# Kernel optimization log

Hardware: AMD Instinct MI355X
Metric: run time of the kernel (lower is better)

Reference implementation:

```python
import jax, jax.numpy as jnp
import numpy as np


def setup_inputs() -> dict:
    key = jax.random.key(0)
    ks = jax.random.split(key, 8)
    B, N, D, H = 8, 512, 64, 64
    user_embeddings = jax.random.normal(ks[0], (B, N, D), dtype=jnp.float32)
    past_lengths = jax.random.randint(ks[1], (B,), 0, N)
    valid_mask = jnp.ones((B, N), dtype=jnp.float32)
    # MLP params: Linear(4D -> H), PReLU (single slope), Linear(H -> 1)
    s1 = 1.0 / np.sqrt(4 * D)
    s2 = 1.0 / np.sqrt(H)
    W1 = jax.random.uniform(ks[2], (H, 4 * D), minval=-s1, maxval=s1, dtype=jnp.float32)
    b1 = jax.random.uniform(ks[3], (H,), minval=-s1, maxval=s1, dtype=jnp.float32)
    prelu_a = jnp.float32(0.25)
    W2 = jax.random.uniform(ks[4], (1, H), minval=-s2, maxval=s2, dtype=jnp.float32)
    b2 = jax.random.uniform(ks[5], (1,), minval=-s2, maxval=s2, dtype=jnp.float32)
    return {"past_lengths": past_lengths, "user_embeddings": user_embeddings,
            "valid_mask": valid_mask, "W1": W1, "b1": b1, "prelu_a": prelu_a,
            "W2": W2, "b2": b2}


def reference(past_lengths, user_embeddings, valid_mask, W1, b1, prelu_a, W2, b2):
    # DIN local activation attention with causal mask.
    # Original math: h = W1 @ concat(Q, K, Q-K, Q*K) + b1 per (q,k) pair.
    # Split W1 into its 4 D-sized blocks so the concat tensor [B,N,N,4D] is
    # never materialized; the pairwise hidden [B,N,N,H] is the only big buffer.
    B, N, D = user_embeddings.shape
    Wq, Wk, Wd, Wm = jnp.split(W1, 4, axis=1)  # each [H, D]
    x = user_embeddings
    # Q and (Q-K)'s +Q part -> per-query term; K and (Q-K)'s -K part -> per-key term
    hq = jnp.einsum('bqd,hd->bqh', x, Wq + Wd)          # [B,N,H]
    hk = jnp.einsum('bkd,hd->bkh', x, Wk - Wd)          # [B,N,H]
    hm = jnp.einsum('bqd,bkd,hd->bqkh', x, x, Wm)       # [B,N,N,H] (Q*K term)
    h = hq[:, :, None, :] + hk[:, None, :, :] + hm + b1
    h = jnp.where(h > 0, h, prelu_a * h)                # PReLU
    scores = jnp.einsum('bqkh,h->bqk', h, W2[0]) + b2[0]  # [B,N,N]
    causal = jnp.tril(jnp.ones((N, N), dtype=scores.dtype))
    scores = scores * causal[None, :, :]
    scores = scores * valid_mask[:, None, :]            # key-side padding mask
    encoded = jnp.einsum('bqk,bkd->bqd', scores, x)     # weighted sum (no softmax)
    return encoded
```

## Files before the change

kernel.cpp:

```cpp
#include <hip/hip_runtime.h>

#define NB 8
#define NN 512

#define WS_WMF 0
#define WS_HQ  4096
#define WS_BF  266240
#define WS_XE  528384

typedef float fx4 __attribute__((ext_vector_type(4)));
typedef short sx8 __attribute__((ext_vector_type(8)));
typedef int   ix4 __attribute__((ext_vector_type(4)));

static __device__ inline unsigned short f2bf(float f) {
    unsigned u = __float_as_uint(f);
    return (unsigned short)((u + 0x7FFFu + ((u >> 16) & 1u)) >> 16);
}

static __device__ inline void async_cp16(const void* g, void* l) {
    __builtin_amdgcn_global_load_lds(
        (const __attribute__((address_space(1))) unsigned int*)g,
        (__attribute__((address_space(3))) unsigned int*)l, 16, 0, 0);
}

__global__ __launch_bounds__(256) void prep(const float* __restrict__ x,
                                            const float* __restrict__ vm,
                                            const float* __restrict__ W1,
                                            const float* __restrict__ b1,
                                            float* __restrict__ ws) {
    __shared__ float lwq[64 * 68];
    __shared__ float lwk[64 * 68];
    __shared__ float xs[1024];
    const int t = threadIdx.x;
    const int blk = blockIdx.x;

    {
        int d = t & 63, hb = t >> 6;
        #pragma unroll 4
        for (int i = 0; i < 16; ++i) {
            int h = i * 4 + hb;
            float a = W1[h * 256 + d];
            float bb = W1[h * 256 + 64 + d];
            float c = W1[h * 256 + 128 + d];
            lwq[h * 68 + d] = a + c;
            lwk[h * 68 + d] = bb - c;
        }
    }
    const int r0 = blk * 16;
    #pragma unroll
    for (int i = 0; i < 4; ++i)
        xs[i * 256 + t] = x[r0 * 64 + i * 256 + t];
    __syncthreads();

    {
        int r4 = t >> 6, h = t & 63;
        const fx4* wqv = (const fx4*)(lwq + h * 68);
        const fx4* wkv = (const fx4*)(lwk + h * 68);
        float bh = b1[h];
        unsigned short* bfp = (unsigned short*)(ws + WS_BF);
        #pragma unroll 1
        for (int g = 0; g < 4; ++g) {
            int r = g * 4 + r4;
            const fx4* xr = (const fx4*)(xs + r * 64);
            float aq = bh, ak = 0.f;
            #pragma unroll
            for (int dd = 0; dd < 16; ++dd) {
                fx4 xv = xr[dd];
                fx4 wq = wqv[dd];
                fx4 wk = wkv[dd];
                aq = fmaf(xv[0], wq[0], aq); aq = fmaf(xv[1], wq[1], aq);
                aq = fmaf(xv[2], wq[2], aq); aq = fmaf(xv[3], wq[3], aq);
                ak = fmaf(xv[0], wk[0], ak); ak = fmaf(xv[1], wk[1], ak);
                ak = fmaf(xv[2], wk[2], ak); ak = fmaf(xv[3], wk[3], ak);
            }
            int row = r0 + r;
            (ws + WS_HQ)[row * 64 + h] = aq;
            int bb = row >> 9, k = row & 511;
            int tt = k >> 4, nn = k & 15;
            int c = 2 + (h >> 5);
            int qd = (h >> 3) & 3, j = h & 7;
            int ln = qd * 16 + nn;
            bfp[((((bb * 32 + tt) * 4 + c) * 64 + ln) << 3) + j] = f2bf(ak);
        }
    }

    {
        int b = blk >> 5, t5 = blk & 31;
        if (t < 128) {
            unsigned short* bfp = (unsigned short*)(ws + WS_BF);
            int c = t >> 6, L = t & 63;
            int nn = L & 15, qd = L >> 4;
            const float* src = x + ((b * 512 + t5 * 16 + nn) * 64 + c * 32 + qd * 8);
            fx4 v0 = *(const fx4*)src;
            fx4 v1 = *(const fx4*)(src + 4);
            uint4 o;
            o.x = (unsigned)f2bf(v0[0]) | ((unsigned)f2bf(v0[1]) << 16);
            o.y = (unsigned)f2bf(v0[2]) | ((unsigned)f2bf(v0[3]) << 16);
            o.z = (unsigned)f2bf(v1[0]) | ((unsigned)f2bf(v1[1]) << 16);
            o.w = (unsigned)f2bf(v1[2]) | ((unsigned)f2bf(v1[3]) << 16);
            *(uint4*)(bfp + ((((b * 32 + t5) * 4 + c) * 64 + L) << 3)) = o;
        }
        {
            unsigned short* xep = (unsigned short*)(ws + WS_XE);
            int c32 = t5 >> 1, half = t5 & 1;
            int nt = t >> 6, r = t & 63;
            int L = half * 32 + (r & 31);
            int j0 = (r >> 5) * 4;
            int quad = L >> 4, nn = L & 15;
            unsigned short u[4];
            #pragma unroll
            for (int i = 0; i < 4; ++i) {
                int key = c32 * 32 + quad * 8 + j0 + i;
                float v = x[(b * 512 + key) * 64 + nt * 16 + nn] * vm[b * 512 + key];
                u[i] = f2bf(v);
            }
            uint2 o;
            o.x = (unsigned)u[0] | ((unsigned)u[1] << 16);
            o.y = (unsigned)u[2] | ((unsigned)u[3] << 16);
            *(uint2*)(xep + (((((b * 16 + c32) * 4 + nt) * 64 + L) << 3) + j0)) = o;
        }
    }
    if (blk < 2) {
        float* wmf = ws + WS_WMF;
        int e = blk * 256 + t;
        int slot = e >> 6, lane = e & 63;
        int ht = slot >> 1, hf = slot & 1;
        int mm = lane & 15, qd = lane >> 4;
        int h = ht * 16 + mm;
        int dbase = hf * 32 + qd * 8;
        #pragma unroll
        for (int j = 0; j < 8; ++j)
            wmf[e * 8 + j] = W1[h * 256 + 192 + dbase + j];
    }
}

__global__ __launch_bounds__(256, 2) void k2_main(const float* __restrict__ x,
                                                  const float* __restrict__ prelu_a,
                                                  const float* __restrict__ W2,
                                                  const float* __restrict__ b2,
                                                  const float* __restrict__ ws,
                                                  float* __restrict__ out) {
    const int tid  = threadIdx.x;
    const int lane = tid & 63;
    const int w    = tid >> 6;
    const int blk  = blockIdx.x;
    const int band = (int)((0x4501763298DCABEFULL >> ((blk >> 6) << 2)) & 0xF);
    const int rest = blk & 63;
    const int b    = rest >> 3;
    const int s    = rest & 7;
    const int n    = lane & 15, quad = lane >> 4;
    const int q    = band * 32 + s * 4 + w;
    const int bq   = b * 512 + q;
    const int cmax = band;

    const float* wmf = ws + WS_WMF;
    const float* hq  = ws + WS_HQ;
    const unsigned short* bfp = (const unsigned short*)(ws + WS_BF);
    const unsigned short* xep = (const unsigned short*)(ws + WS_XE);

    const float pa  = prelu_a[0];
    const float b2v = b2[0];

    __shared__ uint4 bufS[2][512];
    __shared__ unsigned strip[4][16];

    fx4 w2v[4];
    #pragma unroll
    for (int ht = 0; ht < 4; ++ht)
        w2v[ht] = *(const fx4*)(W2 + ht * 16 + quad * 4);
    sx8 oh[4];
    #pragma unroll
    for (int ht = 0; ht < 4; ++ht) {
        sx8 a;
        #pragma unroll
        for (int jj = 0; jj < 8; ++jj) {
            int hp = (ht >> 1) * 32 + quad * 8 + jj;
            a[jj] = (hp == ht * 16 + n) ? (short)0x3F80 : (short)0;
        }
        oh[ht] = a;
    }
    const unsigned sel = (quad < 2) ? 0x05040100u : 0x07060302u;

    fx4 hqv[4];
    #pragma unroll
    for (int ht = 0; ht < 4; ++ht)
        hqv[ht] = *(const fx4*)(hq + bq * 64 + ht * 16 + quad * 4);
    float xq[2][8];
    {
        const float* xp = x + bq * 64 + quad * 8;
        fx4 t0 = *(const fx4*)xp;
        fx4 t1 = *(const fx4*)(xp + 4);
        fx4 t2 = *(const fx4*)(xp + 32);
        fx4 t3 = *(const fx4*)(xp + 36);
        #pragma unroll
        for (int jj = 0; jj < 4; ++jj) {
            xq[0][jj] = t0[jj]; xq[0][4 + jj] = t1[jj];
            xq[1][jj] = t2[jj]; xq[1][4 + jj] = t3[jj];
        }
    }
    sx8 afrag[4][2];
    #pragma unroll
    for (int ht = 0; ht < 4; ++ht)
        #pragma unroll
        for (int hf = 0; hf < 2; ++hf) {
            const float* wp = wmf + (((ht * 2 + hf) * 64 + lane) << 3);
            fx4 w0 = *(const fx4*)wp;
            fx4 w1 = *(const fx4*)(wp + 4);
            sx8 a;
            #pragma unroll
            for (int jj = 0; jj < 4; ++jj) {
                a[jj]     = (short)f2bf(w0[jj] * xq[hf][jj]);
                a[4 + jj] = (short)f2bf(w1[jj] * xq[hf][4 + jj]);
            }
            afrag[ht][hf] = a;
        }

    fx4 eacc[4];
    #pragma unroll
    for (int nt = 0; nt < 4; ++nt) eacc[nt] = (fx4){0.f, 0.f, 0.f, 0.f};

    {
        const uint4* sS = (const uint4*)(bfp + (unsigned)(b * 32) * 2048);
        async_cp16(sS + tid,       &bufS[0][tid]);
        async_cp16(sS + tid + 256, &bufS[0][tid + 256]);
    }
    __syncthreads();

    #pragma unroll 1
    for (int c = 0; c <= cmax; ++c) {
        if (c < cmax) {
            const int p2 = (c + 1) & 1;
            const uint4* sS = (const uint4*)(bfp + (unsigned)(b * 32 + 2 * (c + 1)) * 2048);
            async_cp16(sS + tid,       &bufS[p2][tid]);
            async_cp16(sS + tid + 256, &bufS[p2][tid + 256]);
        }

        const int p = c & 1;
        const unsigned short* ls = (const unsigned short*)&bufS[p][0] + (lane << 3);
        sx8 fa0 = *(const sx8*)(ls);
        sx8 fa1 = *(const sx8*)(ls + 512);
        sx8 fa2 = *(const sx8*)(ls + 1024);
        sx8 fa3 = *(const sx8*)(ls + 1536);
        sx8 fb0 = *(const sx8*)(ls + 2048);
        sx8 fb1 = *(const sx8*)(ls + 2560);
        sx8 fb2 = *(const sx8*)(ls + 3072);
        sx8 fb3 = *(const sx8*)(ls + 3584);

        fx4 accA[4], accB[4];
        #pragma unroll
        for (int ht = 0; ht < 4; ++ht) { accA[ht] = hqv[ht]; accB[ht] = hqv[ht]; }
        #pragma unroll
        for (int ht = 0; ht < 4; ++ht) {
            accA[ht] = __builtin_amdgcn_mfma_f32_16x16x32_bf16(afrag[ht][0], fa0, accA[ht], 0, 0, 0);
            accB[ht] = __builtin_amdgcn_mfma_f32_16x16x32_bf16(afrag[ht][0], fb0, accB[ht], 0, 0, 0);
        }
        #pragma unroll
        for (int ht = 0; ht < 4; ++ht) {
            accA[ht] = __builtin_amdgcn_mfma_f32_16x16x32_bf16(afrag[ht][1], fa1, accA[ht], 0, 0, 0);
            accB[ht] = __builtin_amdgcn_mfma_f32_16x16x32_bf16(afrag[ht][1], fb1, accB[ht], 0, 0, 0);
        }
        #pragma unroll
        for (int ht = 0; ht < 4; ++ht) {
            accA[ht] = __builtin_amdgcn_mfma_f32_16x16x32_bf16(oh[ht], (ht < 2) ? fa2 : fa3, accA[ht], 0, 0, 0);
            accB[ht] = __builtin_amdgcn_mfma_f32_16x16x32_bf16(oh[ht], (ht < 2) ? fb2 : fb3, accB[ht], 0, 0, 0);
        }

        const unsigned short* le = xep + ((unsigned)(b * 16 + c) * 2048) + (lane << 3);
        sx8 e0 = *(const sx8*)(le);
        sx8 e1 = *(const sx8*)(le + 512);
        sx8 e2 = *(const sx8*)(le + 1024);
        sx8 e3 = *(const sx8*)(le + 1536);

        fx4 s0v = (fx4){0.f, 0.f, 0.f, 0.f};
        fx4 s1v = (fx4){0.f, 0.f, 0.f, 0.f};
        #pragma unroll
        for (int ht = 0; ht < 4; ++ht) {
            fx4 za = accA[ht], zb = accB[ht];
            fx4 ta = __builtin_elementwise_max(za, za * pa);
            fx4 tb = __builtin_elementwise_max(zb, zb * pa);
            s0v = ta * w2v[ht] + s0v;
            s1v = tb * w2v[ht] + s1v;
        }
        float s0 = (s0v[0] + s0v[1]) + (s0v[2] + s0v[3]);
        float s1 = (s1v[0] + s1v[1]) + (s1v[2] + s1v[3]);
        s0 += __shfl_xor(s0, 16, 64);
        s0 += __shfl_xor(s0, 32, 64);
        s1 += __shfl_xor(s1, 16, 64);
        s1 += __shfl_xor(s1, 32, 64);
        int k0 = c * 32 + n;
        s0 = (k0 <= q)      ? s0 + b2v : 0.f;
        s1 = (k0 + 16 <= q) ? s1 + b2v : 0.f;

        unsigned packed = (unsigned)f2bf(s0) | ((unsigned)f2bf(s1) << 16);
        if (quad == 0) strip[w][n] = packed;
        const unsigned* sp = &strip[w][(quad & 1) * 8];
        uint4 wv0 = *(const uint4*)sp;
        uint4 wv1 = *(const uint4*)(sp + 4);
        ix4 sw_;
        sw_[0] = (int)__builtin_amdgcn_perm(wv0.y, wv0.x, sel);
        sw_[1] = (int)__builtin_amdgcn_perm(wv0.w, wv0.z, sel);
        sw_[2] = (int)__builtin_amdgcn_perm(wv1.y, wv1.x, sel);
        sw_[3] = (int)__builtin_amdgcn_perm(wv1.w, wv1.z, sel);
        sx8 sfrag = __builtin_bit_cast(sx8, sw_);

        eacc[0] = __builtin_amdgcn_mfma_f32_16x16x32_bf16(sfrag, e0, eacc[0], 0, 0, 0);
        eacc[1] = __builtin_amdgcn_mfma_f32_16x16x32_bf16(sfrag, e1, eacc[1], 0, 0, 0);
        eacc[2] = __builtin_amdgcn_mfma_f32_16x16x32_bf16(sfrag, e2, eacc[2], 0, 0, 0);
        eacc[3] = __builtin_amdgcn_mfma_f32_16x16x32_bf16(sfrag, e3, eacc[3], 0, 0, 0);

        __syncthreads();
    }

    float ov = eacc[0][0];
    if (quad == 1) ov = eacc[1][0];
    if (quad == 2) ov = eacc[2][0];
    if (quad == 3) ov = eacc[3][0];
    out[bq * 64 + lane] = ov;
}

extern "C" void kernel_launch(void* const* d_in, const int* in_sizes, int n_in,
                              void* d_out, int out_size, void* d_ws, size_t ws_size,
                              hipStream_t stream) {
    const float* x   = (const float*)d_in[1];
    const float* vmk = (const float*)d_in[2];
    const float* W1  = (const float*)d_in[3];
    const float* b1  = (const float*)d_in[4];
    const float* pa  = (const float*)d_in[5];
    const float* W2  = (const float*)d_in[6];
    const float* b2  = (const float*)d_in[7];
    float* ws  = (float*)d_ws;
    float* out = (float*)d_out;

    hipLaunchKernelGGL(prep, dim3(256), dim3(256), 0, stream,
                       x, vmk, W1, b1, ws);
    hipLaunchKernelGGL(k2_main, dim3(1024), dim3(256), 0, stream,
                       x, pa, W2, b2, ws, out);
}
```

Measured before the change: 99.66 us.

## Replace LDS double-buffered key fragments with register double-buffering

Removes the shared-memory staging buffer and async global-to-LDS copies for per-chunk key fragments. Each wave now loads its fragments straight from global memory into registers, ping-ponging between two register arrays over an unrolled-by-two loop. The per-iteration __syncthreads is dropped. This cuts LDS traffic and block-wide barriers, at the cost of higher VGPR pressure and each wave loading the same data independently (redundant global/L2 traffic).

```diff
diff --git a/kernel.cpp b/kernel.cpp
--- a/kernel.cpp
+++ b/kernel.cpp
@@ -15,12 +15,6 @@
 static __device__ inline unsigned short f2bf(float f) {
     unsigned u = __float_as_uint(f);
     return (unsigned short)((u + 0x7FFFu + ((u >> 16) & 1u)) >> 16);
-}
-
-static __device__ inline void async_cp16(const void* g, void* l) {
-    __builtin_amdgcn_global_load_lds(
-        (const __attribute__((address_space(1))) unsigned int*)g,
-        (__attribute__((address_space(3))) unsigned int*)l, 16, 0, 0);
 }
 
 __global__ __launch_bounds__(256) void prep(const float* __restrict__ x,
@@ -161,7 +155,6 @@
     const float pa  = prelu_a[0];
     const float b2v = b2[0];
 
-    __shared__ uint4 bufS[2][512];
     __shared__ unsigned strip[4][16];
 
     fx4 w2v[4];
@@ -219,53 +212,33 @@
     #pragma unroll
     for (int nt = 0; nt < 4; ++nt) eacc[nt] = (fx4){0.f, 0.f, 0.f, 0.f};
 
-    {
-        const uint4* sS = (const uint4*)(bfp + (unsigned)(b * 32) * 2048);
-        async_cp16(sS + tid,       &bufS[0][tid]);
-        async_cp16(sS + tid + 256, &bufS[0][tid + 256]);
-    }
-    __syncthreads();
-
-    #pragma unroll 1
-    for (int c = 0; c <= cmax; ++c) {
-        if (c < cmax) {
-            const int p2 = (c + 1) & 1;
-            const uint4* sS = (const uint4*)(bfp + (unsigned)(b * 32 + 2 * (c + 1)) * 2048);
-            async_cp16(sS + tid,       &bufS[p2][tid]);
-            async_cp16(sS + tid + 256, &bufS[p2][tid + 256]);
-        }
-
-        const int p = c & 1;
-        const unsigned short* ls = (const unsigned short*)&bufS[p][0] + (lane << 3);
-        sx8 fa0 = *(const sx8*)(ls);
-        sx8 fa1 = *(const sx8*)(ls + 512);
-        sx8 fa2 = *(const sx8*)(ls + 1024);
-        sx8 fa3 = *(const sx8*)(ls + 1536);
-        sx8 fb0 = *(const sx8*)(ls + 2048);
-        sx8 fb1 = *(const sx8*)(ls + 2560);
-        sx8 fb2 = *(const sx8*)(ls + 3072);
-        sx8 fb3 = *(const sx8*)(ls + 3584);
+    auto round = [&](int cc, sx8 (&cur)[8], sx8 (&nxt)[8]) {
+        if (cc < cmax) {
+            const sx8* sp_ = (const sx8*)bfp + ((unsigned)(b * 32 + 2 * (cc + 1)) << 8);
+            #pragma unroll
+            for (int g = 0; g < 8; ++g) nxt[g] = sp_[(g << 6) + lane];
+        }
 
         fx4 accA[4], accB[4];
         #pragma unroll
         for (int ht = 0; ht < 4; ++ht) { accA[ht] = hqv[ht]; accB[ht] = hqv[ht]; }
         #pragma unroll
         for (int ht = 0; ht < 4; ++ht) {
-            accA[ht] = __builtin_amdgcn_mfma_f32_16x16x32_bf16(afrag[ht][0], fa0, accA[ht], 0, 0, 0);
-            accB[ht] = __builtin_amdgcn_mfma_f32_16x16x32_bf16(afrag[ht][0], fb0, accB[ht], 0, 0, 0);
+            accA[ht] = __builtin_amdgcn_mfma_f32_16x16x32_bf16(afrag[ht][0], cur[0], accA[ht], 0, 0, 0);
+            accB[ht] = __builtin_amdgcn_mfma_f32_16x16x32_bf16(afrag[ht][0], cur[4], accB[ht], 0, 0, 0);
         }
         #pragma unroll
         for (int ht = 0; ht < 4; ++ht) {
-            accA[ht] = __builtin_amdgcn_mfma_f32_16x16x32_bf16(afrag[ht][1], fa1, accA[ht], 0, 0, 0);
-            accB[ht] = __builtin_amdgcn_mfma_f32_16x16x32_bf16(afrag[ht][1], fb1, accB[ht], 0, 0, 0);
+            accA[ht] = __builtin_amdgcn_mfma_f32_16x16x32_bf16(afrag[ht][1], cur[1], accA[ht], 0, 0, 0);
+            accB[ht] = __builtin_amdgcn_mfma_f32_16x16x32_bf16(afrag[ht][1], cur[5], accB[ht], 0, 0, 0);
         }
         #pragma unroll
         for (int ht = 0; ht < 4; ++ht) {
-            accA[ht] = __builtin_amdgcn_mfma_f32_16x16x32_bf16(oh[ht], (ht < 2) ? fa2 : fa3, accA[ht], 0, 0, 0);
-            accB[ht] = __builtin_amdgcn_mfma_f32_16x16x32_bf16(oh[ht], (ht < 2) ? fb2 : fb3, accB[ht], 0, 0, 0);
-        }
-
-        const unsigned short* le = xep + ((unsigned)(b * 16 + c) * 2048) + (lane << 3);
+            accA[ht] = __builtin_amdgcn_mfma_f32_16x16x32_bf16(oh[ht], (ht < 2) ? cur[2] : cur[3], accA[ht], 0, 0, 0);
+            accB[ht] = __builtin_amdgcn_mfma_f32_16x16x32_bf16(oh[ht], (ht < 2) ? cur[6] : cur[7], accB[ht], 0, 0, 0);
+        }
+
+        const unsigned short* le = xep + ((unsigned)(b * 16 + cc) * 2048) + (lane << 3);
         sx8 e0 = *(const sx8*)(le);
         sx8 e1 = *(const sx8*)(le + 512);
         sx8 e2 = *(const sx8*)(le + 1024);
@@ -287,7 +260,7 @@
         s0 += __shfl_xor(s0, 32, 64);
         s1 += __shfl_xor(s1, 16, 64);
         s1 += __shfl_xor(s1, 32, 64);
-        int k0 = c * 32 + n;
+        int k0 = cc * 32 + n;
         s0 = (k0 <= q)      ? s0 + b2v : 0.f;
         s1 = (k0 + 16 <= q) ? s1 + b2v : 0.f;
 
@@ -307,8 +280,18 @@
         eacc[1] = __builtin_amdgcn_mfma_f32_16x16x32_bf16(sfrag, e1, eacc[1], 0, 0, 0);
         eacc[2] = __builtin_amdgcn_mfma_f32_16x16x32_bf16(sfrag, e2, eacc[2], 0, 0, 0);
         eacc[3] = __builtin_amdgcn_mfma_f32_16x16x32_bf16(sfrag, e3, eacc[3], 0, 0, 0);
-
-        __syncthreads();
+    };
+
+    sx8 frA[8], frB[8];
+    {
+        const sx8* sp_ = (const sx8*)bfp + ((unsigned)(b * 32) << 8);
+        #pragma unroll
+        for (int g = 0; g < 8; ++g) frA[g] = sp_[(g << 6) + lane];
+    }
+    #pragma unroll 1
+    for (int c = 0; c <= cmax; c += 2) {
+        round(c, frA, frB);
+        if (c + 1 <= cmax) round(c + 1, frB, frA);
     }
 
     float ov = eacc[0][0];
```

Result: no change. 101.0 us (+1.3%).
